# Kernel tuning notes

Hardware: AMD Instinct MI355X
Metric: run time of the kernel (lower is better)

## Reference

```python
import jax, jax.numpy as jnp
import numpy as np

B, T, C = 16, 1024, 1024
VOCAB = 32000


def setup_inputs() -> dict:
    key = jax.random.key(0)
    ks = jax.random.split(key, 12)
    s = 0.02
    inp = {
        "x": jax.random.normal(ks[0], (B, T, C), dtype=jnp.float32),
        "idx": jax.random.randint(ks[1], (B, T), 0, VOCAB),
        "Wk": jax.random.normal(ks[2], (C, C), dtype=jnp.float32) * s,
        "bk": jnp.zeros((C,), dtype=jnp.float32),
        "Wq": jax.random.normal(ks[3], (C, C), dtype=jnp.float32) * s,
        "bq": jnp.zeros((C,), dtype=jnp.float32),
        "Wv": jax.random.normal(ks[4], (C, C), dtype=jnp.float32) * s,
        "bv": jnp.zeros((C,), dtype=jnp.float32),
        "Wp": jax.random.normal(ks[5], (C, C), dtype=jnp.float32) * s,
        "bp": jnp.zeros((C,), dtype=jnp.float32),
        "ang_emb": jax.random.normal(ks[6], (VOCAB, C // 2), dtype=jnp.float32) * s,
    }
    return inp


def reference(x, idx, Wk, bk, Wq, bq, Wv, bv, Wp, bp, ang_emb):
    Bv, Tv, Cv = x.shape
    # projections (torch Linear: x @ W.T + b)
    k = x @ Wk.T + bk
    q = x @ Wq.T + bq
    v = x @ Wv.T + bv
    # reversed cumulative angle sum per token: angle[t] = sum_{s>=t} emb[idx[s]]
    angle = ang_emb[idx]  # [B,T,C/2]
    angle = jnp.flip(jnp.cumsum(jnp.flip(angle, axis=1), axis=1), axis=1)
    cos_a, sin_a = jnp.cos(angle), jnp.sin(angle)  # [B,T,C/2]

    def rot(z):  # apply [[cos,-sin],[sin,cos]] to channel pairs
        z = z.reshape(Bv, Tv, Cv // 2, 2)
        z0, z1 = z[..., 0], z[..., 1]
        return jnp.stack([cos_a * z0 - sin_a * z1,
                          sin_a * z0 + cos_a * z1], axis=-1).reshape(Bv, Tv, Cv)

    def inv_rot(z):  # transpose of the rotation matrix
        z = z.reshape(Bv, Tv, Cv // 2, 2)
        z0, z1 = z[..., 0], z[..., 1]
        return jnp.stack([cos_a * z0 + sin_a * z1,
                          -sin_a * z0 + cos_a * z1], axis=-1).reshape(Bv, Tv, Cv)

    k = rot(k)
    q = rot(q)
    v = rot(v)  # primed=True
    # NOTE: original computes k @ q^T (not q @ k^T)
    wei = jnp.einsum("btc,bsc->bts", k, q) * (Cv ** -0.5)
    causal = jnp.tril(jnp.ones((Tv, Tv), dtype=bool))
    # softplus attention; masked (-inf) entries -> softplus(-inf) = 0
    wei = jnp.where(causal, jax.nn.softplus(wei), jnp.zeros((), wei.dtype))
    out = jnp.einsum("bts,bsc->btc", wei, v)
    out = inv_rot(out)  # primed=True
    out = out @ Wp.T + bp
    return out
```

## Files before the change

### kernel.cpp

```cpp
#include <hip/hip_runtime.h>
#include <math.h>

typedef unsigned short u16;
typedef unsigned int u32;
typedef __bf16 bf16x8 __attribute__((ext_vector_type(8)));
typedef float f32x4 __attribute__((ext_vector_type(4)));

__device__ __forceinline__ u16 f2b(float f) {
    u32 u = __float_as_uint(f);
    return (u16)((u + 0x7FFFu + ((u >> 16) & 1u)) >> 16);
}
__device__ __forceinline__ float b2f(u16 h) {
    return __uint_as_float(((u32)h) << 16);
}

#define GLL16(gp, lp)                                                          \
    __builtin_amdgcn_global_load_lds(                                          \
        (__attribute__((address_space(1))) void*)(const_cast<u16*>(gp)),       \
        (__attribute__((address_space(3))) void*)(lp), 16, 0, 0)

template <int EPI, int MODE>
__global__ __launch_bounds__(512, 2) void gemm256(
    const u16* __restrict__ A, long long sAz,
    const u16* __restrict__ B, long long sBz,
    void* __restrict__ D0, void* __restrict__ D1, void* __restrict__ D2,
    long long sDz,
    const float* __restrict__ bias0, const float* __restrict__ bias1,
    const float* __restrict__ bias2,
    const u32* __restrict__ cossin,
    int N, int K, float scale, int WB)
{
    extern __shared__ u16 lds[];
    u16* const As = lds;
    u16* const Bs = lds + 2 * 256 * 64;

    int bx, by, bz;
    if (MODE == 0) {
        const int n = blockIdx.x;
        const int xcd = n & 7, m = n >> 3;
        by = xcd + 8 * (m / WB);
        bx = m % WB;
        bz = 0;
    } else if (MODE == 1) {
        const int n = blockIdx.x;
        bz = n & 15;
        const int t = n >> 4;
        by = (t >= 1) + (t >= 3) + (t >= 6);
        bx = t - ((by * (by + 1)) >> 1);
    } else {
        const int n = blockIdx.x;
        bz = n & 15;
        const int t = n >> 4;
        by = t >> 2;
        bx = t & 3;
    }
    const int r0 = by * 256, c0 = bx * 256;

    const int kEnd = (MODE == 2) ? (((by + 1) * 256) < K ? ((by + 1) * 256) : K) : K;
    const int nkt = kEnd >> 6;

    const int tid = threadIdx.x;
    const int lane = tid & 63, wave = tid >> 6;
    const int wr = wave >> 2, wc = wave & 3;

    const u16* __restrict__ Ab = A + (long long)bz * sAz + (long long)r0 * K;
    const u16* __restrict__ Bb = B + (long long)bz * sBz + (long long)c0 * K;

    const int srow = tid >> 3;
    const int skc8 = (((tid & 7) ^ ((tid >> 4) & 7))) * 8;

    const int lr = lane & 15;
    const int xr = (lane >> 1) & 7;
    const int kof0 = (((lane >> 4) + 0) ^ xr) * 8;
    const int kof1 = (((lane >> 4) + 4) ^ xr) * 8;

    f32x4 acc[8][4];
    #pragma unroll
    for (int i = 0; i < 8; ++i)
        #pragma unroll
        for (int j = 0; j < 4; ++j)
            acc[i][j] = (f32x4){0.f, 0.f, 0.f, 0.f};

    #pragma unroll
    for (int r = 0; r < 4; ++r)
        GLL16(Bb + (long long)(r * 64 + srow) * K + skc8, Bs + r * 4096 + tid * 8);
    GLL16(Ab + (long long)(0 * 64 + srow) * K + skc8, As + 0 * 4096 + tid * 8);
    GLL16(Ab + (long long)(2 * 64 + srow) * K + skc8, As + 2 * 4096 + tid * 8);
    GLL16(Ab + (long long)(1 * 64 + srow) * K + skc8, As + 1 * 4096 + tid * 8);
    GLL16(Ab + (long long)(3 * 64 + srow) * K + skc8, As + 3 * 4096 + tid * 8);
    asm volatile("s_waitcnt vmcnt(2)" ::: "memory");
    __builtin_amdgcn_s_barrier();

    for (int kt = 0; kt < nkt; ++kt) {
        const int buf = kt & 1;
        const u16* asb = As + buf * 16384;
        const u16* bsb = Bs + buf * 16384;
        u16* asn = As + (buf ^ 1) * 16384;
        u16* bsn = Bs + (buf ^ 1) * 16384;
        const long long kbn = (long long)(kt + 1) * 64 + skc8;
        const bool pf = (kt + 1 < nkt);
        bf16x8 bc[2][4];
        #pragma unroll
        for (int ph = 0; ph < 2; ++ph) {
            const int rq = ph;
            const int ab0 = wr * 128 + rq * 64;
            bf16x8 a0[4], a1[4];
            #pragma unroll
            for (int i = 0; i < 4; ++i) {
                const int row = (ab0 + i * 16 + lr) * 64;
                a0[i] = *(const bf16x8*)&asb[row + kof0];
                a1[i] = *(const bf16x8*)&asb[row + kof1];
            }
            if (rq == 0) {
                #pragma unroll
                for (int j = 0; j < 4; ++j) {
                    const int row = (wc * 64 + j * 16 + lr) * 64;
                    bc[0][j] = *(const bf16x8*)&bsb[row + kof0];
                    bc[1][j] = *(const bf16x8*)&bsb[row + kof1];
                }
            }
            if (pf) {
                if (ph == 0) {
                    GLL16(Ab + (long long)(0 * 64 + srow) * K + kbn, asn + 0 * 4096 + tid * 8);
                    GLL16(Ab + (long long)(2 * 64 + srow) * K + kbn, asn + 2 * 4096 + tid * 8);
                    GLL16(Bb + (long long)(0 * 64 + srow) * K + kbn, bsn + 0 * 4096 + tid * 8);
                    GLL16(Bb + (long long)(1 * 64 + srow) * K + kbn, bsn + 1 * 4096 + tid * 8);
                } else {
                    GLL16(Bb + (long long)(2 * 64 + srow) * K + kbn, bsn + 2 * 4096 + tid * 8);
                    GLL16(Bb + (long long)(3 * 64 + srow) * K + kbn, bsn + 3 * 4096 + tid * 8);
                    GLL16(Ab + (long long)(1 * 64 + srow) * K + kbn, asn + 1 * 4096 + tid * 8);
                    GLL16(Ab + (long long)(3 * 64 + srow) * K + kbn, asn + 3 * 4096 + tid * 8);
                }
            }
            asm volatile("s_waitcnt lgkmcnt(0)" ::: "memory");
            __builtin_amdgcn_sched_barrier(0);
            __builtin_amdgcn_s_setprio(1);
            #pragma unroll
            for (int i = 0; i < 4; ++i)
                #pragma unroll
                for (int j = 0; j < 4; ++j) {
                    acc[rq * 4 + i][j] = __builtin_amdgcn_mfma_f32_16x16x32_bf16(
                        a0[i], bc[0][j], acc[rq * 4 + i][j], 0, 0, 0);
                    acc[rq * 4 + i][j] = __builtin_amdgcn_mfma_f32_16x16x32_bf16(
                        a1[i], bc[1][j], acc[rq * 4 + i][j], 0, 0, 0);
                }
            __builtin_amdgcn_s_setprio(0);
            if (ph == 0) {
                if (pf) asm volatile("s_waitcnt vmcnt(4)" ::: "memory");
                else    asm volatile("s_waitcnt vmcnt(0)" ::: "memory");
            } else if (pf) {
                asm volatile("s_waitcnt vmcnt(2)" ::: "memory");
            }
            __builtin_amdgcn_s_barrier();
        }
    }

    void* Dp = D0;
    const float* bp_ = bias0;
    int ldD = N, cbase = c0, sel = 0;
    if (EPI == 0) {
        sel = bx >> 2;
        Dp  = (sel == 0) ? D0 : (sel == 1) ? D1 : D2;
        bp_ = (sel == 0) ? bias0 : (sel == 1) ? bias1 : bias2;
        ldD = 1024;
        cbase = c0 & 1023;
    }

    const int rl = (lane >> 4) * 4, cl = lane & 15;
    const int grb = r0 + wr * 128;
    const int gcb = cbase + wc * 64;

    if (EPI == 0 && sel == 2) {
        #pragma unroll
        for (int ai = 0; ai < 8; ++ai) {
            #pragma unroll
            for (int bj = 0; bj < 4; ++bj) {
                const int gr0 = grb + ai * 16 + rl;
                const int gcd = gcb + bj * 16 + cl;
                u16 pk[4];
                #pragma unroll
                for (int v = 0; v < 4; ++v) {
                    const int gr = gr0 + v;
                    float my = acc[ai][bj][v] + bp_[gcd];
                    float other = __shfl_xor(my, 1);
                    u32 csn = cossin[(long long)gr * 512 + (gcd >> 1)];
                    float cs = b2f((u16)(csn & 0xffff)), sn = b2f((u16)(csn >> 16));
                    float res = (gcd & 1) ? (sn * other + cs * my)
                                          : (cs * my - sn * other);
                    pk[v] = f2b(res);
                }
                const int bb = gr0 >> 10, tt = gr0 & 1023;
                u16* dst = (u16*)Dp + ((((long long)bb << 10) + gcd) << 10) + tt;
                uint2 pw;
                pw.x = (u32)pk[0] | ((u32)pk[1] << 16);
                pw.y = (u32)pk[2] | ((u32)pk[3] << 16);
                *(uint2*)dst = pw;
            }
        }
        return;
    }

    #pragma unroll
    for (int ai = 0; ai < 8; ++ai) {
        #pragma unroll
        for (int bj = 0; bj < 4; ++bj) {
            const int gr0 = grb + ai * 16 + rl;
            const int gcd = gcb + bj * 16 + cl;
            #pragma unroll
            for (int v = 0; v < 4; ++v) {
                const int gr = gr0 + v;
                float val = acc[ai][bj][v];
                const long long o = (long long)bz * sDz + (long long)gr * ldD + gcd;
                if (EPI == 0) {
                    float my = val + bp_[gcd];
                    float other = __shfl_xor(my, 1);
                    u32 csn = cossin[(long long)gr * 512 + (gcd >> 1)];
                    float cs = b2f((u16)(csn & 0xffff)), sn = b2f((u16)(csn >> 16));
                    float res = (gcd & 1) ? (sn * other + cs * my)
                                          : (cs * my - sn * other);
                    ((u16*)Dp)[o] = f2b(res);
                } else if (EPI == 1) {
                    float xs = val * scale;
                    float r = (gcd <= gr) ? ((xs > 15.f) ? xs : log1pf(__expf(xs))) : 0.f;
                    ((u16*)Dp)[o] = f2b(r);
                } else if (EPI == 2) {
                    float my = val;
                    float other = __shfl_xor(my, 1);
                    u32 csn = cossin[((long long)((bz << 10) + gr)) * 512 + (gcd >> 1)];
                    float cs = b2f((u16)(csn & 0xffff)), sn = b2f((u16)(csn >> 16));
                    float res = (gcd & 1) ? (cs * my - sn * other)
                                          : (cs * my + sn * other);
                    ((u16*)Dp)[o] = f2b(res);
                } else {
                    ((float*)Dp)[o] = val + bp_[gcd];
                }
            }
        }
    }
}

__global__ void f2b_kern(const float* __restrict__ in, u16* __restrict__ out, int n4) {
    int i = blockIdx.x * blockDim.x + threadIdx.x;
    if (i >= n4) return;
    float4 f = ((const float4*)in)[i];
    uint2 o;
    o.x = (u32)f2b(f.x) | ((u32)f2b(f.y) << 16);
    o.y = (u32)f2b(f.z) | ((u32)f2b(f.w) << 16);
    ((uint2*)out)[i] = o;
}

__global__ void f2b_w4(const float* __restrict__ a, const float* __restrict__ b,
                       const float* __restrict__ c, const float* __restrict__ d,
                       u16* __restrict__ oa, u16* __restrict__ ob,
                       u16* __restrict__ oc, u16* __restrict__ od, int n4) {
    int i = blockIdx.x * blockDim.x + threadIdx.x;
    if (i >= n4) return;
    const float* src = (blockIdx.y == 0) ? a : (blockIdx.y == 1) ? b
                     : (blockIdx.y == 2) ? c : d;
    u16* dst = (blockIdx.y == 0) ? oa : (blockIdx.y == 1) ? ob
             : (blockIdx.y == 2) ? oc : od;
    float4 f = ((const float4*)src)[i];
    uint2 o;
    o.x = (u32)f2b(f.x) | ((u32)f2b(f.y) << 16);
    o.y = (u32)f2b(f.z) | ((u32)f2b(f.w) << 16);
    ((uint2*)dst)[i] = o;
}

#define TT 1024
#define CC2 512
#define NCH 32
#define CL 32

__global__ void angle_partial(const int* __restrict__ idx, const float* __restrict__ emb,
                              float* __restrict__ partial) {
    int b = blockIdx.x >> 5, ch = blockIdx.x & 31;
    int c = threadIdx.x;
    float s = 0.f;
    int tb = ch * CL;
    for (int t = 0; t < CL; t++) {
        int row = idx[b * TT + tb + t];
        s += emb[(long long)row * CC2 + c];
    }
    partial[((long long)b * NCH + ch) * CC2 + c] = s;
}

__global__ void angle_final(const int* __restrict__ idx, const float* __restrict__ emb,
                            const float* __restrict__ partial,
                            u32* __restrict__ cossin) {
    int b = blockIdx.x >> 5, ch = blockIdx.x & 31;
    int c = threadIdx.x;
    float run = 0.f;
    for (int cc = NCH - 1; cc > ch; cc--)
        run += partial[((long long)b * NCH + cc) * CC2 + c];
    for (int t = CL - 1; t >= 0; t--) {
        int tt = ch * CL + t;
        int row = idx[b * TT + tt];
        run += emb[(long long)row * CC2 + c];
        float sn, cs;
        __sincosf(run, &sn, &cs);
        cossin[((long long)b * TT + tt) * CC2 + c] = (u32)f2b(cs) | ((u32)f2b(sn) << 16);
    }
}

extern "C" void kernel_launch(void* const* d_in, const int* in_sizes, int n_in,
                              void* d_out, int out_size, void* d_ws, size_t ws_size,
                              hipStream_t stream) {
    const int Bn = 16, T = 1024, C = 1024;
    const long long TC = (long long)T * C;
    const size_t nx = (size_t)Bn * T * C;
    const size_t npairs = nx / 2;

    const float* x   = (const float*)d_in[0];
    const int*   idx = (const int*)d_in[1];
    const float* Wk  = (const float*)d_in[2];
    const float* bk  = (const float*)d_in[3];
    const float* Wq  = (const float*)d_in[4];
    const float* bq  = (const float*)d_in[5];
    const float* Wv  = (const float*)d_in[6];
    const float* bv  = (const float*)d_in[7];
    const float* Wp  = (const float*)d_in[8];
    const float* bp  = (const float*)d_in[9];
    const float* emb = (const float*)d_in[10];
    float* out = (float*)d_out;

    static bool s_attr = false;
    if (!s_attr) {
        auto* k0 = gemm256<0, 0>;
        auto* k1 = gemm256<1, 1>;
        auto* k2 = gemm256<2, 2>;
        auto* k3 = gemm256<3, 0>;
        (void)hipFuncSetAttribute(reinterpret_cast<const void*>(k0),
                                  hipFuncAttributeMaxDynamicSharedMemorySize, 131072);
        (void)hipFuncSetAttribute(reinterpret_cast<const void*>(k1),
                                  hipFuncAttributeMaxDynamicSharedMemorySize, 131072);
        (void)hipFuncSetAttribute(reinterpret_cast<const void*>(k2),
                                  hipFuncAttributeMaxDynamicSharedMemorySize, 131072);
        (void)hipFuncSetAttribute(reinterpret_cast<const void*>(k3),
                                  hipFuncAttributeMaxDynamicSharedMemorySize, 131072);
        s_attr = true;
    }

    u16* xb  = (u16*)d_ws;
    u16* kb  = xb + nx;
    u16* qb  = kb + nx;
    u16* vT  = qb + nx;
    u32* cossin = (u32*)(vT + nx);
    u16* Wall = (u16*)(cossin + npairs);
    u16* Wpb  = Wall + (size_t)3 * C * C;
    float* partial = (float*)(Wpb + (size_t)C * C);
    u16* wei = xb;

    f2b_kern<<<(int)(nx / 4 / 256), 256, 0, stream>>>(x, xb, (int)(nx / 4));
    f2b_w4<<<dim3(C * C / 4 / 256, 4), 256, 0, stream>>>(
        Wk, Wq, Wv, Wp, Wall, Wall + (size_t)C * C, Wall + (size_t)2 * C * C, Wpb,
        C * C / 4);

    angle_partial<<<Bn * NCH, 512, 0, stream>>>(idx, emb, partial);
    angle_final<<<Bn * NCH, 512, 0, stream>>>(idx, emb, partial, cossin);

    gemm256<0, 0><<<768, 512, 131072, stream>>>(
        xb, 0, Wall, 0, kb, qb, vT, 0, bk, bq, bv, cossin,
        3 * C, C, 1.f, 12);

    gemm256<1, 1><<<160, 512, 131072, stream>>>(
        kb, TC, qb, TC, wei, nullptr, nullptr, (long long)T * T,
        nullptr, nullptr, nullptr, nullptr, T, C, 0.03125f, 0);

    gemm256<2, 2><<<256, 512, 131072, stream>>>(
        wei, (long long)T * T, vT, (long long)C * T, qb, nullptr, nullptr, TC,
        nullptr, nullptr, nullptr, cossin, C, T, 1.f, 0);

    gemm256<3, 0><<<256, 512, 131072, stream>>>(
        qb, 0, Wpb, 0, out, nullptr, nullptr, 0, bp, nullptr, nullptr, nullptr,
        C, C, 1.f, 4);
}
```

Baseline: 466.3 us.

## Split GEMM k-tile into four quadrant phases with interleaved prefetch and barriers

```diff
diff --git a/kernel.cpp b/kernel.cpp
--- a/kernel.cpp
+++ b/kernel.cpp
@@ -99,56 +99,64 @@
         u16* bsn = Bs + (buf ^ 1) * 16384;
         const long long kbn = (long long)(kt + 1) * 64 + skc8;
         const bool pf = (kt + 1 < nkt);
-        bf16x8 bc[2][4];
+        bf16x8 a0[4], a1[4];
+        bf16x8 b0[2][2], b1[2][2];
         #pragma unroll
-        for (int ph = 0; ph < 2; ++ph) {
-            const int rq = ph;
-            const int ab0 = wr * 128 + rq * 64;
-            bf16x8 a0[4], a1[4];
-            #pragma unroll
-            for (int i = 0; i < 4; ++i) {
-                const int row = (ab0 + i * 16 + lr) * 64;
-                a0[i] = *(const bf16x8*)&asb[row + kof0];
-                a1[i] = *(const bf16x8*)&asb[row + kof1];
-            }
-            if (rq == 0) {
+        for (int q = 0; q < 4; ++q) {
+            const int rq = q >> 1, cq = q & 1;
+            if (cq == 0) {
+                const int ab0 = wr * 128 + rq * 64;
                 #pragma unroll
-                for (int j = 0; j < 4; ++j) {
-                    const int row = (wc * 64 + j * 16 + lr) * 64;
-                    bc[0][j] = *(const bf16x8*)&bsb[row + kof0];
-                    bc[1][j] = *(const bf16x8*)&bsb[row + kof1];
+                for (int i = 0; i < 4; ++i) {
+                    const int row = (ab0 + i * 16 + lr) * 64;
+                    a0[i] = *(const bf16x8*)&asb[row + kof0];
+                    a1[i] = *(const bf16x8*)&asb[row + kof1];
+                }
+            }
+            if (q < 2) {
+                const int bb0r = wc * 64 + q * 32;
+                #pragma unroll
+                for (int j = 0; j < 2; ++j) {
+                    const int row = (bb0r + j * 16 + lr) * 64;
+                    b0[q][j] = *(const bf16x8*)&bsb[row + kof0];
+                    b1[q][j] = *(const bf16x8*)&bsb[row + kof1];
                 }
             }
             if (pf) {
-                if (ph == 0) {
+                if (q == 0) {
+                    GLL16(Bb + (long long)(0 * 64 + srow) * K + kbn, bsn + 0 * 4096 + tid * 8);
+                    GLL16(Bb + (long long)(1 * 64 + srow) * K + kbn, bsn + 1 * 4096 + tid * 8);
+                } else if (q == 1) {
+                    GLL16(Bb + (long long)(2 * 64 + srow) * K + kbn, bsn + 2 * 4096 + tid * 8);
+                    GLL16(Bb + (long long)(3 * 64 + srow) * K + kbn, bsn + 3 * 4096 + tid * 8);
+                } else if (q == 2) {
                     GLL16(Ab + (long long)(0 * 64 + srow) * K + kbn, asn + 0 * 4096 + tid * 8);
                     GLL16(Ab + (long long)(2 * 64 + srow) * K + kbn, asn + 2 * 4096 + tid * 8);
-                    GLL16(Bb + (long long)(0 * 64 + srow) * K + kbn, bsn + 0 * 4096 + tid * 8);
-                    GLL16(Bb + (long long)(1 * 64 + srow) * K + kbn, bsn + 1 * 4096 + tid * 8);
                 } else {
-                    GLL16(Bb + (long long)(2 * 64 + srow) * K + kbn, bsn + 2 * 4096 + tid * 8);
-                    GLL16(Bb + (long long)(3 * 64 + srow) * K + kbn, bsn + 3 * 4096 + tid * 8);
                     GLL16(Ab + (long long)(1 * 64 + srow) * K + kbn, asn + 1 * 4096 + tid * 8);
                     GLL16(Ab + (long long)(3 * 64 + srow) * K + kbn, asn + 3 * 4096 + tid * 8);
                 }
             }
+            if (q == 0)
+                asm volatile("s_waitcnt lgkmcnt(8)" ::: "memory");
+            __builtin_amdgcn_s_barrier();
             asm volatile("s_waitcnt lgkmcnt(0)" ::: "memory");
             __builtin_amdgcn_sched_barrier(0);
             __builtin_amdgcn_s_setprio(1);
             #pragma unroll
             for (int i = 0; i < 4; ++i)
                 #pragma unroll
-                for (int j = 0; j < 4; ++j) {
-                    acc[rq * 4 + i][j] = __builtin_amdgcn_mfma_f32_16x16x32_bf16(
-                        a0[i], bc[0][j], acc[rq * 4 + i][j], 0, 0, 0);
-                    acc[rq * 4 + i][j] = __builtin_amdgcn_mfma_f32_16x16x32_bf16(
-                        a1[i], bc[1][j], acc[rq * 4 + i][j], 0, 0, 0);
+                for (int j = 0; j < 2; ++j) {
+                    acc[rq * 4 + i][cq * 2 + j] = __builtin_amdgcn_mfma_f32_16x16x32_bf16(
+                        a0[i], b0[cq][j], acc[rq * 4 + i][cq * 2 + j], 0, 0, 0);
+                    acc[rq * 4 + i][cq * 2 + j] = __builtin_amdgcn_mfma_f32_16x16x32_bf16(
+                        a1[i], b1[cq][j], acc[rq * 4 + i][cq * 2 + j], 0, 0, 0);
                 }
             __builtin_amdgcn_s_setprio(0);
-            if (ph == 0) {
+            if (q == 1) {
                 if (pf) asm volatile("s_waitcnt vmcnt(4)" ::: "memory");
                 else    asm volatile("s_waitcnt vmcnt(0)" ::: "memory");
-            } else if (pf) {
+            } else if (q == 3 && pf) {
                 asm volatile("s_waitcnt vmcnt(2)" ::: "memory");
             }
             __builtin_amdgcn_s_barrier();
```

Result: slower. 591.2 us (+26.8%).

## Stage GEMM epilogue through LDS for vectorized stores; merge prep kernels

Applied to the files above, without the earlier changes.

```diff
diff --git a/kernel.cpp b/kernel.cpp
--- a/kernel.cpp
+++ b/kernel.cpp
@@ -200,70 +200,99 @@
         return;
     }
 
-    #pragma unroll
-    for (int ai = 0; ai < 8; ++ai) {
+    {
+        float* slab = (float*)lds + (size_t)wave * (16 * 68);
         #pragma unroll
-        for (int bj = 0; bj < 4; ++bj) {
-            const int gr0 = grb + ai * 16 + rl;
-            const int gcd = gcb + bj * 16 + cl;
+        for (int ai = 0; ai < 8; ++ai) {
             #pragma unroll
-            for (int v = 0; v < 4; ++v) {
-                const int gr = gr0 + v;
-                float val = acc[ai][bj][v];
-                const long long o = (long long)bz * sDz + (long long)gr * ldD + gcd;
+            for (int bj = 0; bj < 4; ++bj)
+                #pragma unroll
+                for (int v = 0; v < 4; ++v)
+                    slab[(rl + v) * 68 + bj * 16 + cl] = acc[ai][bj][v];
+            asm volatile("s_waitcnt lgkmcnt(0)" ::: "memory");
+            #pragma unroll
+            for (int half = 0; half < 2; ++half) {
+                const int rloc = half * 8 + (lane >> 3);
+                const int c0l  = (lane & 7) * 8;
+                const int gr   = grb + ai * 16 + rloc;
+                const int gcd0 = gcb + c0l;
+                float v8[8];
+                #pragma unroll
+                for (int e = 0; e < 8; ++e)
+                    v8[e] = slab[rloc * 68 + c0l + e];
+                const long long o = (long long)bz * sDz + (long long)gr * ldD + gcd0;
                 if (EPI == 0) {
-                    float my = val + bp_[gcd];
-                    float other = __shfl_xor(my, 1);
-                    u32 csn = cossin[(long long)gr * 512 + (gcd >> 1)];
-                    float cs = b2f((u16)(csn & 0xffff)), sn = b2f((u16)(csn >> 16));
-                    float res = (gcd & 1) ? (sn * other + cs * my)
-                                          : (cs * my - sn * other);
-                    ((u16*)Dp)[o] = f2b(res);
+                    const float4 ba = *(const float4*)&bp_[gcd0];
+                    const float4 bbv = *(const float4*)&bp_[gcd0 + 4];
+                    const float bb8[8] = {ba.x, ba.y, ba.z, ba.w,
+                                          bbv.x, bbv.y, bbv.z, bbv.w};
+                    const uint4 cs4 = *(const uint4*)&cossin[(long long)gr * 512 + (gcd0 >> 1)];
+                    const u32 csw[4] = {cs4.x, cs4.y, cs4.z, cs4.w};
+                    u16 pk[8];
+                    #pragma unroll
+                    for (int p = 0; p < 4; ++p) {
+                        const float e0 = v8[2 * p] + bb8[2 * p];
+                        const float e1 = v8[2 * p + 1] + bb8[2 * p + 1];
+                        const float cs = b2f((u16)(csw[p] & 0xffff));
+                        const float sn = b2f((u16)(csw[p] >> 16));
+                        pk[2 * p]     = f2b(cs * e0 - sn * e1);
+                        pk[2 * p + 1] = f2b(sn * e0 + cs * e1);
+                    }
+                    uint4 pw;
+                    pw.x = (u32)pk[0] | ((u32)pk[1] << 16);
+                    pw.y = (u32)pk[2] | ((u32)pk[3] << 16);
+                    pw.z = (u32)pk[4] | ((u32)pk[5] << 16);
+                    pw.w = (u32)pk[6] | ((u32)pk[7] << 16);
+                    *(uint4*)&((u16*)Dp)[o] = pw;
                 } else if (EPI == 1) {
-                    float xs = val * scale;
-                    float r = (gcd <= gr) ? ((xs > 15.f) ? xs : log1pf(__expf(xs))) : 0.f;
-                    ((u16*)Dp)[o] = f2b(r);
+                    u16 pk[8];
+                    #pragma unroll
+                    for (int e = 0; e < 8; ++e) {
+                        const float xs = v8[e] * scale;
+                        const float r = ((gcd0 + e) <= gr)
+                            ? ((xs > 15.f) ? xs : log1pf(__expf(xs))) : 0.f;
+                        pk[e] = f2b(r);
+                    }
+                    uint4 pw;
+                    pw.x = (u32)pk[0] | ((u32)pk[1] << 16);
+                    pw.y = (u32)pk[2] | ((u32)pk[3] << 16);
+                    pw.z = (u32)pk[4] | ((u32)pk[5] << 16);
+                    pw.w = (u32)pk[6] | ((u32)pk[7] << 16);
+                    *(uint4*)&((u16*)Dp)[o] = pw;
                 } else if (EPI == 2) {
-                    float my = val;
-                    float other = __shfl_xor(my, 1);
-                    u32 csn = cossin[((long long)((bz << 10) + gr)) * 512 + (gcd >> 1)];
-                    float cs = b2f((u16)(csn & 0xffff)), sn = b2f((u16)(csn >> 16));
-                    float res = (gcd & 1) ? (cs * my - sn * other)
-                                          : (cs * my + sn * other);
-                    ((u16*)Dp)[o] = f2b(res);
+                    const uint4 cs4 = *(const uint4*)
+                        &cossin[((long long)((bz << 10) + gr)) * 512 + (gcd0 >> 1)];
+                    const u32 csw[4] = {cs4.x, cs4.y, cs4.z, cs4.w};
+                    u16 pk[8];
+                    #pragma unroll
+                    for (int p = 0; p < 4; ++p) {
+                        const float e0 = v8[2 * p], e1 = v8[2 * p + 1];
+                        const float cs = b2f((u16)(csw[p] & 0xffff));
+                        const float sn = b2f((u16)(csw[p] >> 16));
+                        pk[2 * p]     = f2b(cs * e0 + sn * e1);
+                        pk[2 * p + 1] = f2b(cs * e1 - sn * e0);
+                    }
+                    uint4 pw;
+                    pw.x = (u32)pk[0] | ((u32)pk[1] << 16);
+                    pw.y = (u32)pk[2] | ((u32)pk[3] << 16);
+                    pw.z = (u32)pk[4] | ((u32)pk[5] << 16);
+                    pw.w = (u32)pk[6] | ((u32)pk[7] << 16);
+                    *(uint4*)&((u16*)Dp)[o] = pw;
                 } else {
-                    ((float*)Dp)[o] = val + bp_[gcd];
+                    const float4 ba = *(const float4*)&bp_[gcd0];
+                    const float4 bbv = *(const float4*)&bp_[gcd0 + 4];
+                    float4 s0, s1;
+                    s0.x = v8[0] + ba.x;  s0.y = v8[1] + ba.y;
+                    s0.z = v8[2] + ba.z;  s0.w = v8[3] + ba.w;
+                    s1.x = v8[4] + bbv.x; s1.y = v8[5] + bbv.y;
+                    s1.z = v8[6] + bbv.z; s1.w = v8[7] + bbv.w;
+                    *(float4*)&((float*)Dp)[o]     = s0;
+                    *(float4*)&((float*)Dp)[o + 4] = s1;
                 }
             }
+            asm volatile("s_waitcnt lgkmcnt(0)" ::: "memory");
         }
     }
-}
-
-__global__ void f2b_kern(const float* __restrict__ in, u16* __restrict__ out, int n4) {
-    int i = blockIdx.x * blockDim.x + threadIdx.x;
-    if (i >= n4) return;
-    float4 f = ((const float4*)in)[i];
-    uint2 o;
-    o.x = (u32)f2b(f.x) | ((u32)f2b(f.y) << 16);
-    o.y = (u32)f2b(f.z) | ((u32)f2b(f.w) << 16);
-    ((uint2*)out)[i] = o;
-}
-
-__global__ void f2b_w4(const float* __restrict__ a, const float* __restrict__ b,
-                       const float* __restrict__ c, const float* __restrict__ d,
-                       u16* __restrict__ oa, u16* __restrict__ ob,
-                       u16* __restrict__ oc, u16* __restrict__ od, int n4) {
-    int i = blockIdx.x * blockDim.x + threadIdx.x;
-    if (i >= n4) return;
-    const float* src = (blockIdx.y == 0) ? a : (blockIdx.y == 1) ? b
-                     : (blockIdx.y == 2) ? c : d;
-    u16* dst = (blockIdx.y == 0) ? oa : (blockIdx.y == 1) ? ob
-             : (blockIdx.y == 2) ? oc : od;
-    float4 f = ((const float4*)src)[i];
-    uint2 o;
-    o.x = (u32)f2b(f.x) | ((u32)f2b(f.y) << 16);
-    o.y = (u32)f2b(f.z) | ((u32)f2b(f.w) << 16);
-    ((uint2*)dst)[i] = o;
 }
 
 #define TT 1024
@@ -271,17 +300,48 @@
 #define NCH 32
 #define CL 32
 
-__global__ void angle_partial(const int* __restrict__ idx, const float* __restrict__ emb,
-                              float* __restrict__ partial) {
-    int b = blockIdx.x >> 5, ch = blockIdx.x & 31;
-    int c = threadIdx.x;
-    float s = 0.f;
-    int tb = ch * CL;
-    for (int t = 0; t < CL; t++) {
-        int row = idx[b * TT + tb + t];
-        s += emb[(long long)row * CC2 + c];
-    }
-    partial[((long long)b * NCH + ch) * CC2 + c] = s;
+__global__ void prep(const float* __restrict__ x,
+                     const float* __restrict__ Wk, const float* __restrict__ Wq,
+                     const float* __restrict__ Wv, const float* __restrict__ Wp,
+                     u16* __restrict__ xb, u16* __restrict__ wall,
+                     u16* __restrict__ wpb,
+                     const int* __restrict__ idx, const float* __restrict__ emb,
+                     float* __restrict__ partial)
+{
+    const int bid = blockIdx.x, tid = threadIdx.x;
+    if (bid < 16384) {
+        const int i = bid * 256 + tid;
+        float4 f = ((const float4*)x)[i];
+        uint2 o;
+        o.x = (u32)f2b(f.x) | ((u32)f2b(f.y) << 16);
+        o.y = (u32)f2b(f.z) | ((u32)f2b(f.w) << 16);
+        ((uint2*)xb)[i] = o;
+    } else if (bid < 20480) {
+        const int s = bid - 16384;
+        const int w = s >> 10;
+        const int i = (s & 1023) * 256 + tid;
+        const float* src = (w == 0) ? Wk : (w == 1) ? Wq : (w == 2) ? Wv : Wp;
+        u16* dst = (w == 0) ? wall : (w == 1) ? wall + 1024 * 1024
+                 : (w == 2) ? wall + 2 * 1024 * 1024 : wpb;
+        float4 f = ((const float4*)src)[i];
+        uint2 o;
+        o.x = (u32)f2b(f.x) | ((u32)f2b(f.y) << 16);
+        o.y = (u32)f2b(f.z) | ((u32)f2b(f.w) << 16);
+        ((uint2*)dst)[i] = o;
+    } else {
+        const int s = bid - 20480;
+        const int b = s >> 6;
+        const int r = s & 63;
+        const int ch = r >> 1, half = r & 1;
+        const int c = half * 256 + tid;
+        float acc = 0.f;
+        const int tb = ch * CL;
+        for (int t = 0; t < CL; t++) {
+            const int row = idx[b * TT + tb + t];
+            acc += emb[(long long)row * CC2 + c];
+        }
+        partial[((long long)b * NCH + ch) * CC2 + c] = acc;
+    }
 }
 
 __global__ void angle_final(const int* __restrict__ idx, const float* __restrict__ emb,
@@ -350,12 +410,9 @@
     float* partial = (float*)(Wpb + (size_t)C * C);
     u16* wei = xb;
 
-    f2b_kern<<<(int)(nx / 4 / 256), 256, 0, stream>>>(x, xb, (int)(nx / 4));
-    f2b_w4<<<dim3(C * C / 4 / 256, 4), 256, 0, stream>>>(
-        Wk, Wq, Wv, Wp, Wall, Wall + (size_t)C * C, Wall + (size_t)2 * C * C, Wpb,
-        C * C / 4);
-
-    angle_partial<<<Bn * NCH, 512, 0, stream>>>(idx, emb, partial);
+    prep<<<21504, 256, 0, stream>>>(x, Wk, Wq, Wv, Wp, xb, Wall, Wpb,
+                                    idx, emb, partial);
+
     angle_final<<<Bn * NCH, 512, 0, stream>>>(idx, emb, partial, cossin);
 
     gemm256<0, 0><<<768, 512, 131072, stream>>>(
```

After: 492.9 us. 1.06x slower.

## Use 128x128 tile GEMM for attention stages and fuse prep kernels

Applied to the files above, without the earlier changes.

```diff
diff --git a/kernel.cpp b/kernel.cpp
--- a/kernel.cpp
+++ b/kernel.cpp
@@ -6,6 +6,10 @@
 typedef __bf16 bf16x8 __attribute__((ext_vector_type(8)));
 typedef float f32x4 __attribute__((ext_vector_type(4)));
 
+#define BM 128
+#define BN 128
+#define BK 32
+
 __device__ __forceinline__ u16 f2b(float f) {
     u32 u = __float_as_uint(f);
     return (u16)((u + 0x7FFFu + ((u >> 16) & 1u)) >> 16);
@@ -18,6 +22,115 @@
     __builtin_amdgcn_global_load_lds(                                          \
         (__attribute__((address_space(1))) void*)(const_cast<u16*>(gp)),       \
         (__attribute__((address_space(3))) void*)(lp), 16, 0, 0)
+
+template <int EPI, bool EARLY, bool KLIM, int SWZ, bool SPLIT>
+__global__ __launch_bounds__(256) void gemm_nt(
+    const u16* __restrict__ A, long long sAz,
+    const u16* __restrict__ B, long long sBz,
+    void* __restrict__ D0, void* __restrict__ D1, void* __restrict__ D2,
+    long long sDz,
+    const float* __restrict__ bias0, const float* __restrict__ bias1,
+    const float* __restrict__ bias2,
+    const u32* __restrict__ cossin,
+    int M, int N, int K, float scale, int WB)
+{
+    int bx, by, bz;
+    {
+        const int n = blockIdx.x;
+        const int xcd = n & 7, m = n >> 3;
+        if (SWZ == 0) {
+            by = xcd + 8 * (m / WB);
+            bx = m % WB;
+            bz = 0;
+        } else {
+            bz = xcd + 8 * (m / WB);
+            const int w = m % WB;
+            bx = w & 7;
+            by = w >> 3;
+        }
+    }
+    const int r0 = by * BM, c0 = bx * BN;
+
+    if (EARLY && c0 >= r0 + BM) return;
+
+    __shared__ __align__(16) u16 As[BM * BK];
+    __shared__ __align__(16) u16 Bs[BN * BK];
+
+    const int tid = threadIdx.x;
+    const int lane = tid & 63, wave = tid >> 6;
+    const int wm = (wave >> 1) * 64, wn = (wave & 1) * 64;
+
+    const u16* Ab = A + (long long)bz * sAz + (long long)r0 * K;
+    const u16* Bb = B + (long long)bz * sBz + (long long)c0 * K;
+
+    const int ra0 = tid >> 2;
+    const int ca0 = (tid & 3) * 8;
+
+    f32x4 acc[4][4];
+    #pragma unroll
+    for (int i = 0; i < 4; i++)
+        #pragma unroll
+        for (int j = 0; j < 4; j++)
+            acc[i][j] = (f32x4){0.f, 0.f, 0.f, 0.f};
+
+    const int kEnd = KLIM ? ((r0 + BM) < K ? (r0 + BM) : K) : K;
+
+    for (int k0 = 0; k0 < kEnd; k0 += BK) {
+        GLL16(Ab + (long long)ra0 * K + k0 + ca0,        &As[tid * 8]);
+        GLL16(Ab + (long long)(ra0 + 64) * K + k0 + ca0, &As[(tid + 256) * 8]);
+        GLL16(Bb + (long long)ra0 * K + k0 + ca0,        &Bs[tid * 8]);
+        GLL16(Bb + (long long)(ra0 + 64) * K + k0 + ca0, &Bs[(tid + 256) * 8]);
+        __syncthreads();
+
+        bf16x8 af[4], bfv[4];
+        #pragma unroll
+        for (int i = 0; i < 4; i++) {
+            af[i]  = *(const bf16x8*)&As[(wm + i * 16 + (lane & 15)) * BK + (lane >> 4) * 8];
+            bfv[i] = *(const bf16x8*)&Bs[(wn + i * 16 + (lane & 15)) * BK + (lane >> 4) * 8];
+        }
+        #pragma unroll
+        for (int i = 0; i < 4; i++)
+            #pragma unroll
+            for (int j = 0; j < 4; j++)
+                acc[i][j] = __builtin_amdgcn_mfma_f32_16x16x32_bf16(af[i], bfv[j], acc[i][j], 0, 0, 0);
+        __syncthreads();
+    }
+
+    void* Dp = D0;
+    int ldD = N;
+    const int cbase = c0;
+
+    const int rl = (lane >> 4) * 4, cl = lane & 15;
+
+    #pragma unroll
+    for (int i = 0; i < 4; i++) {
+        #pragma unroll
+        for (int j = 0; j < 4; j++) {
+            const int gr0 = r0 + wm + i * 16 + rl;
+            const int gc  = wn + j * 16 + cl;
+            const int gcd = cbase + gc;
+            #pragma unroll
+            for (int v = 0; v < 4; v++) {
+                const int gr = gr0 + v;
+                float val = acc[i][j][v];
+                const long long o = (long long)bz * sDz + (long long)gr * ldD + gcd;
+                if (EPI == 1) {
+                    float xs = val * scale;
+                    float r = (gcd <= gr) ? ((xs > 15.f) ? xs : __logf(1.f + __expf(xs))) : 0.f;
+                    ((u16*)Dp)[o] = f2b(r);
+                } else if (EPI == 2) {
+                    float my = val;
+                    float other = __shfl_xor(my, 1);
+                    u32 csn = cossin[((long long)((bz << 10) + gr)) * 512 + (gcd >> 1)];
+                    float cs = b2f((u16)(csn & 0xffff)), sn = b2f((u16)(csn >> 16));
+                    float res = (gcd & 1) ? (cs * my - sn * other)
+                                          : (cs * my + sn * other);
+                    ((u16*)Dp)[o] = f2b(res);
+                }
+            }
+        }
+    }
+}
 
 template <int EPI, int MODE>
 __global__ __launch_bounds__(512, 2) void gemm256(
@@ -35,29 +148,16 @@
     u16* const Bs = lds + 2 * 256 * 64;
 
     int bx, by, bz;
-    if (MODE == 0) {
+    {
         const int n = blockIdx.x;
         const int xcd = n & 7, m = n >> 3;
         by = xcd + 8 * (m / WB);
         bx = m % WB;
         bz = 0;
-    } else if (MODE == 1) {
-        const int n = blockIdx.x;
-        bz = n & 15;
-        const int t = n >> 4;
-        by = (t >= 1) + (t >= 3) + (t >= 6);
-        bx = t - ((by * (by + 1)) >> 1);
-    } else {
-        const int n = blockIdx.x;
-        bz = n & 15;
-        const int t = n >> 4;
-        by = t >> 2;
-        bx = t & 3;
     }
     const int r0 = by * 256, c0 = bx * 256;
 
-    const int kEnd = (MODE == 2) ? (((by + 1) * 256) < K ? ((by + 1) * 256) : K) : K;
-    const int nkt = kEnd >> 6;
+    const int nkt = K >> 6;
 
     const int tid = threadIdx.x;
     const int lane = tid & 63, wave = tid >> 6;
@@ -210,7 +310,7 @@
             for (int v = 0; v < 4; ++v) {
                 const int gr = gr0 + v;
                 float val = acc[ai][bj][v];
-                const long long o = (long long)bz * sDz + (long long)gr * ldD + gcd;
+                const long long o = (long long)gr * ldD + gcd;
                 if (EPI == 0) {
                     float my = val + bp_[gcd];
                     float other = __shfl_xor(my, 1);
@@ -219,51 +319,12 @@
                     float res = (gcd & 1) ? (sn * other + cs * my)
                                           : (cs * my - sn * other);
                     ((u16*)Dp)[o] = f2b(res);
-                } else if (EPI == 1) {
-                    float xs = val * scale;
-                    float r = (gcd <= gr) ? ((xs > 15.f) ? xs : log1pf(__expf(xs))) : 0.f;
-                    ((u16*)Dp)[o] = f2b(r);
-                } else if (EPI == 2) {
-                    float my = val;
-                    float other = __shfl_xor(my, 1);
-                    u32 csn = cossin[((long long)((bz << 10) + gr)) * 512 + (gcd >> 1)];
-                    float cs = b2f((u16)(csn & 0xffff)), sn = b2f((u16)(csn >> 16));
-                    float res = (gcd & 1) ? (cs * my - sn * other)
-                                          : (cs * my + sn * other);
-                    ((u16*)Dp)[o] = f2b(res);
                 } else {
                     ((float*)Dp)[o] = val + bp_[gcd];
                 }
             }
         }
     }
-}
-
-__global__ void f2b_kern(const float* __restrict__ in, u16* __restrict__ out, int n4) {
-    int i = blockIdx.x * blockDim.x + threadIdx.x;
-    if (i >= n4) return;
-    float4 f = ((const float4*)in)[i];
-    uint2 o;
-    o.x = (u32)f2b(f.x) | ((u32)f2b(f.y) << 16);
-    o.y = (u32)f2b(f.z) | ((u32)f2b(f.w) << 16);
-    ((uint2*)out)[i] = o;
-}
-
-__global__ void f2b_w4(const float* __restrict__ a, const float* __restrict__ b,
-                       const float* __restrict__ c, const float* __restrict__ d,
-                       u16* __restrict__ oa, u16* __restrict__ ob,
-                       u16* __restrict__ oc, u16* __restrict__ od, int n4) {
-    int i = blockIdx.x * blockDim.x + threadIdx.x;
-    if (i >= n4) return;
-    const float* src = (blockIdx.y == 0) ? a : (blockIdx.y == 1) ? b
-                     : (blockIdx.y == 2) ? c : d;
-    u16* dst = (blockIdx.y == 0) ? oa : (blockIdx.y == 1) ? ob
-             : (blockIdx.y == 2) ? oc : od;
-    float4 f = ((const float4*)src)[i];
-    uint2 o;
-    o.x = (u32)f2b(f.x) | ((u32)f2b(f.y) << 16);
-    o.y = (u32)f2b(f.z) | ((u32)f2b(f.w) << 16);
-    ((uint2*)dst)[i] = o;
 }
 
 #define TT 1024
@@ -271,17 +332,48 @@
 #define NCH 32
 #define CL 32
 
-__global__ void angle_partial(const int* __restrict__ idx, const float* __restrict__ emb,
-                              float* __restrict__ partial) {
-    int b = blockIdx.x >> 5, ch = blockIdx.x & 31;
-    int c = threadIdx.x;
-    float s = 0.f;
-    int tb = ch * CL;
-    for (int t = 0; t < CL; t++) {
-        int row = idx[b * TT + tb + t];
-        s += emb[(long long)row * CC2 + c];
-    }
-    partial[((long long)b * NCH + ch) * CC2 + c] = s;
+__global__ void prep(const float* __restrict__ x,
+                     const float* __restrict__ Wk, const float* __restrict__ Wq,
+                     const float* __restrict__ Wv, const float* __restrict__ Wp,
+                     u16* __restrict__ xb, u16* __restrict__ wall,
+                     u16* __restrict__ wpb,
+                     const int* __restrict__ idx, const float* __restrict__ emb,
+                     float* __restrict__ partial)
+{
+    const int bid = blockIdx.x, tid = threadIdx.x;
+    if (bid < 16384) {
+        const int i = bid * 256 + tid;
+        float4 f = ((const float4*)x)[i];
+        uint2 o;
+        o.x = (u32)f2b(f.x) | ((u32)f2b(f.y) << 16);
+        o.y = (u32)f2b(f.z) | ((u32)f2b(f.w) << 16);
+        ((uint2*)xb)[i] = o;
+    } else if (bid < 20480) {
+        const int s = bid - 16384;
+        const int w = s >> 10;
+        const int i = (s & 1023) * 256 + tid;
+        const float* src = (w == 0) ? Wk : (w == 1) ? Wq : (w == 2) ? Wv : Wp;
+        u16* dst = (w == 0) ? wall : (w == 1) ? wall + 1024 * 1024
+                 : (w == 2) ? wall + 2 * 1024 * 1024 : wpb;
+        float4 f = ((const float4*)src)[i];
+        uint2 o;
+        o.x = (u32)f2b(f.x) | ((u32)f2b(f.y) << 16);
+        o.y = (u32)f2b(f.z) | ((u32)f2b(f.w) << 16);
+        ((uint2*)dst)[i] = o;
+    } else {
+        const int s = bid - 20480;
+        const int b = s >> 6;
+        const int r = s & 63;
+        const int ch = r >> 1, half = r & 1;
+        const int c = half * 256 + tid;
+        float acc = 0.f;
+        const int tb = ch * CL;
+        for (int t = 0; t < CL; t++) {
+            const int row = idx[b * TT + tb + t];
+            acc += emb[(long long)row * CC2 + c];
+        }
+        partial[((long long)b * NCH + ch) * CC2 + c] = acc;
+    }
 }
 
 __global__ void angle_final(const int* __restrict__ idx, const float* __restrict__ emb,
@@ -326,14 +418,8 @@
     static bool s_attr = false;
     if (!s_attr) {
         auto* k0 = gemm256<0, 0>;
-        auto* k1 = gemm256<1, 1>;
-        auto* k2 = gemm256<2, 2>;
         auto* k3 = gemm256<3, 0>;
         (void)hipFuncSetAttribute(reinterpret_cast<const void*>(k0),
-                                  hipFuncAttributeMaxDynamicSharedMemorySize, 131072);
-        (void)hipFuncSetAttribute(reinterpret_cast<const void*>(k1),
-                                  hipFuncAttributeMaxDynamicSharedMemorySize, 131072);
-        (void)hipFuncSetAttribute(reinterpret_cast<const void*>(k2),
                                   hipFuncAttributeMaxDynamicSharedMemorySize, 131072);
         (void)hipFuncSetAttribute(reinterpret_cast<const void*>(k3),
                                   hipFuncAttributeMaxDynamicSharedMemorySize, 131072);
@@ -350,25 +436,22 @@
     float* partial = (float*)(Wpb + (size_t)C * C);
     u16* wei = xb;
 
-    f2b_kern<<<(int)(nx / 4 / 256), 256, 0, stream>>>(x, xb, (int)(nx / 4));
-    f2b_w4<<<dim3(C * C / 4 / 256, 4), 256, 0, stream>>>(
-        Wk, Wq, Wv, Wp, Wall, Wall + (size_t)C * C, Wall + (size_t)2 * C * C, Wpb,
-        C * C / 4);
-
-    angle_partial<<<Bn * NCH, 512, 0, stream>>>(idx, emb, partial);
+    prep<<<21504, 256, 0, stream>>>(x, Wk, Wq, Wv, Wp, xb, Wall, Wpb,
+                                    idx, emb, partial);
+
     angle_final<<<Bn * NCH, 512, 0, stream>>>(idx, emb, partial, cossin);
 
     gemm256<0, 0><<<768, 512, 131072, stream>>>(
         xb, 0, Wall, 0, kb, qb, vT, 0, bk, bq, bv, cossin,
         3 * C, C, 1.f, 12);
 
-    gemm256<1, 1><<<160, 512, 131072, stream>>>(
+    gemm_nt<1, true, false, 1, false><<<1024, 256, 0, stream>>>(
         kb, TC, qb, TC, wei, nullptr, nullptr, (long long)T * T,
-        nullptr, nullptr, nullptr, nullptr, T, C, 0.03125f, 0);
-
-    gemm256<2, 2><<<256, 512, 131072, stream>>>(
+        nullptr, nullptr, nullptr, nullptr, T, T, C, 0.03125f, 64);
+
+    gemm_nt<2, false, true, 1, false><<<1024, 256, 0, stream>>>(
         wei, (long long)T * T, vT, (long long)C * T, qb, nullptr, nullptr, TC,
-        nullptr, nullptr, nullptr, cossin, C, T, 1.f, 0);
+        nullptr, nullptr, nullptr, cossin, T, C, T, 1.f, 64);
 
     gemm256<3, 0><<<256, 512, 131072, stream>>>(
         qb, 0, Wpb, 0, out, nullptr, nullptr, 0, bp, nullptr, nullptr, nullptr,
```

After: 428.0 us. -8.2%, faster.
